# Performance work log

Measured on AMD Instinct MI355X. Metric: run time of the kernel, lower is better.

The kernel has to match this reference:

```python
import jax, jax.numpy as jnp
import numpy as np

MOVING_RATE = 0.999

def _l2norm(x, eps=1e-12):
    # matches F.normalize(dim=-1): x / max(||x||, eps)
    return x / jnp.maximum(jnp.linalg.norm(x, axis=-1, keepdims=True), eps)

def setup_inputs() -> dict:
    k = jax.random.key(0)
    k1, k2, k3 = jax.random.split(k, 3)
    B, S, K, D = 8192, 14, 512, 256
    return {
        "key": jax.random.normal(k1, (B, S, D), dtype=jnp.float32),
        "value": jax.random.normal(k2, (B, S, D), dtype=jnp.float32),
        "memory": jax.random.normal(k3, (S, K, D), dtype=jnp.float32),
    }

def reference(key, value, memory):
    # key, value: (B, S, D); memory: (S, K, D). update=True path, all slots batched.
    K = memory.shape[1]
    xn = _l2norm(key)                                   # (B,S,D)
    mn = _l2norm(memory)                                # (S,K,D)
    score = jnp.einsum('bsd,skd->bsk', xn, mn)          # (B,S,K)

    # --- EMA codebook update (value is detached in the original) ---
    v = jax.lax.stop_gradient(value)
    ind = jnp.argmax(score, axis=-1)                    # (B,S)
    oh = jax.nn.one_hot(ind, K, dtype=value.dtype)      # (B,S,K)
    oh_sum = oh.sum(axis=0)                             # (S,K)
    emb_sum = jnp.einsum('bsd,bsk->skd', v, oh)         # (S,K,D)
    emb_mean = emb_sum / (oh_sum[..., None] + 1e-6)
    new_mem = memory * MOVING_RATE + emb_mean * (1.0 - MOVING_RATE)

    # --- re-score against updated codebook ---
    score2 = jnp.einsum('bsd,skd->bsk', xn, _l2norm(new_mem))
    ind2 = jnp.argmax(score2, axis=-1)
    oh2 = jax.nn.one_hot(ind2, K, dtype=value.dtype)    # (B,S,K)

    # note: original adds value[:, 0, :] (slot 0) for EVERY slot i — kept faithfully
    out = value[:, :1, :] + jnp.einsum('bsk,skd->bsd', oh2, new_mem)  # (B,S,D)
    return out, new_mem
```

## Files before the change

### kernel.cpp

```cpp
#include <hip/hip_runtime.h>
#include <cstddef>
#include <cstdint>

#define B_ 8192
#define S_ 14
#define K_ 512
#define D_ 256

typedef __attribute__((ext_vector_type(8))) short bfx8;
typedef __attribute__((ext_vector_type(4))) float fx4;

typedef __attribute__((address_space(3))) unsigned int       lds_u32;
typedef const __attribute__((address_space(1))) unsigned int glb_u32;

__device__ __forceinline__ void gload16(const void* g, void* l) {
    __builtin_amdgcn_global_load_lds((glb_u32*)g, (lds_u32*)l, 16, 0, 0);
}

__device__ __forceinline__ unsigned short f2bf(float x) {
    union { float f; unsigned int u; } v; v.f = x;
    unsigned int r = (v.u + 0x7FFFu + ((v.u >> 16) & 1u)) >> 16;
    return (unsigned short)r;
}
__device__ __forceinline__ float bf2f(unsigned short h) {
    union { unsigned int u; float f; } v; v.u = ((unsigned int)h) << 16;
    return v.f;
}

__global__ __launch_bounds__(64) void rownorm_kernel(
    const float* __restrict__ rows, float* __restrict__ invn)
{
    const int row  = blockIdx.x;
    const int lane = threadIdx.x;
    const float4 v = *reinterpret_cast<const float4*>(rows + (size_t)row * D_ + lane * 4);
    float ss = v.x * v.x + v.y * v.y + v.z * v.z + v.w * v.w;
    #pragma unroll
    for (int m = 32; m >= 1; m >>= 1) ss += __shfl_xor(ss, m, 64);
    if (lane == 0) invn[row] = 1.0f / fmaxf(sqrtf(ss), 1e-12f);
}

__global__ __launch_bounds__(256) void split_key_kernel(
    const float* __restrict__ key,
    unsigned short* __restrict__ ph, unsigned short* __restrict__ pm,
    unsigned short* __restrict__ pl)
{
    const int gid  = blockIdx.x * 256 + threadIdx.x;
    const int e    = gid * 4;
    const int b    = e / (S_ * D_);
    const int rem  = e - b * (S_ * D_);
    const int s    = rem >> 8;
    const int d    = rem & 255;
    const float4 x = *reinterpret_cast<const float4*>(key + e);
    const size_t o = ((size_t)s * B_ + b) * D_ + d;

    float xs[4] = { x.x, x.y, x.z, x.w };
    unsigned short hh[4], mm[4], ll[4];
    #pragma unroll
    for (int i = 0; i < 4; ++i) {
        unsigned short a = f2bf(xs[i]);
        float r1 = xs[i] - bf2f(a);
        unsigned short bq = f2bf(r1);
        float r2 = r1 - bf2f(bq);
        unsigned short c = f2bf(r2);
        hh[i] = a; mm[i] = bq; ll[i] = c;
    }
    *reinterpret_cast<ushort4*>(ph + o) = make_ushort4(hh[0], hh[1], hh[2], hh[3]);
    *reinterpret_cast<ushort4*>(pm + o) = make_ushort4(mm[0], mm[1], mm[2], mm[3]);
    *reinterpret_cast<ushort4*>(pl + o) = make_ushort4(ll[0], ll[1], ll[2], ll[3]);
}

__global__ __launch_bounds__(256) void split_mem_kernel(
    const float* __restrict__ mem,
    unsigned short* __restrict__ ph, unsigned short* __restrict__ pm,
    unsigned short* __restrict__ pl)
{
    const int e    = (blockIdx.x * 256 + threadIdx.x) * 4;
    const float4 x = *reinterpret_cast<const float4*>(mem + e);
    float xs[4] = { x.x, x.y, x.z, x.w };
    unsigned short hh[4], mm[4], ll[4];
    #pragma unroll
    for (int i = 0; i < 4; ++i) {
        unsigned short a = f2bf(xs[i]);
        float r1 = xs[i] - bf2f(a);
        unsigned short bq = f2bf(r1);
        float r2 = r1 - bf2f(bq);
        unsigned short c = f2bf(r2);
        hh[i] = a; mm[i] = bq; ll[i] = c;
    }
    *reinterpret_cast<ushort4*>(ph + e) = make_ushort4(hh[0], hh[1], hh[2], hh[3]);
    *reinterpret_cast<ushort4*>(pm + e) = make_ushort4(mm[0], mm[1], mm[2], mm[3]);
    *reinterpret_cast<ushort4*>(pl + e) = make_ushort4(ll[0], ll[1], ll[2], ll[3]);
}

__global__ __launch_bounds__(256) void gemm_argmax_kernel(
    const unsigned short* __restrict__ kh, const unsigned short* __restrict__ km,
    const unsigned short* __restrict__ kl,
    const unsigned short* __restrict__ mh, const unsigned short* __restrict__ mm_,
    const unsigned short* __restrict__ ml,
    const float* __restrict__ invn,
    float* __restrict__ pV, int* __restrict__ pI)
{
    __shared__ short T[6][128 * 32];
    __shared__ float sInv[128];
    __shared__ float bV[128][2];
    __shared__ int   bI[128][2];

    const int orig = blockIdx.x;
    const int wg   = (orig & 7) * 448 + (orig >> 3);
    const int by   = wg & 3;
    const int bx   = (wg >> 2) & 63;
    const int s    = wg >> 8;

    const int t    = threadIdx.x;
    const int b0   = bx * 128;
    const int n0   = by * 128;
    const int w    = t >> 6;
    const int lane = t & 63;
    const int wm   = w >> 1, wn = w & 1;
    const int lr   = lane & 15, lg = lane >> 4;

    const size_t sB = (size_t)s * B_;
    const size_t sK = (size_t)s * K_;

    const unsigned short* __restrict__ APl[3] = { kh, km, kl };
    const unsigned short* __restrict__ BPl[3] = { mh, mm_, ml };

    fx4 acc[4][4];
    #pragma unroll
    for (int i = 0; i < 4; ++i)
        #pragma unroll
        for (int j = 0; j < 4; ++j) acc[i][j] = (fx4)0.0f;

    const int rsub = lane >> 2;
    const int csw  = (((lane & 3) ^ ((lane >> 3) & 3)) * 8);
    const int rdof = ((lg ^ ((lr >> 1) & 3)) * 8);

    for (int dc = 0; dc < 8; ++dc) {
        const int dco = dc * 32 + csw;
        #pragma unroll
        for (int p = 0; p < 3; ++p) {
            #pragma unroll
            for (int u = 0; u < 2; ++u) {
                const int R0 = w * 32 + u * 16;
                gload16(APl[p] + (sB + b0 + R0 + rsub) * D_ + dco, &T[p][R0 * 32]);
                gload16(BPl[p] + (sK + n0 + R0 + rsub) * D_ + dco, &T[3 + p][R0 * 32]);
            }
        }
        __syncthreads();

        #pragma unroll
        for (int ap = 0; ap < 3; ++ap) {
            bfx8 af[4];
            #pragma unroll
            for (int i = 0; i < 4; ++i)
                af[i] = *reinterpret_cast<const bfx8*>(
                    &T[ap][(wm * 64 + i * 16 + lr) * 32 + rdof]);
            #pragma unroll
            for (int bp = 0; bp < 3 - ap; ++bp) {
                bfx8 bfr[4];
                #pragma unroll
                for (int j = 0; j < 4; ++j)
                    bfr[j] = *reinterpret_cast<const bfx8*>(
                        &T[3 + bp][(wn * 64 + j * 16 + lr) * 32 + rdof]);
                __builtin_amdgcn_s_setprio(1);
                #pragma unroll
                for (int i = 0; i < 4; ++i)
                    #pragma unroll
                    for (int j = 0; j < 4; ++j)
                        acc[i][j] = __builtin_amdgcn_mfma_f32_16x16x32_bf16(
                            af[i], bfr[j], acc[i][j], 0, 0, 0);
                __builtin_amdgcn_s_setprio(0);
            }
        }
        __syncthreads();
    }

    if (t < 128) sInv[t] = invn[sK + n0 + t];
    __syncthreads();

    #pragma unroll
    for (int i = 0; i < 4; ++i) {
        #pragma unroll
        for (int r = 0; r < 4; ++r) {
            float bv = -3.4e38f; int bi = 0x7fffffff;
            #pragma unroll
            for (int j = 0; j < 4; ++j) {
                const int kloc = wn * 64 + j * 16 + lr;
                const float v  = acc[i][j][r] * sInv[kloc];
                const int  kg  = n0 + kloc;
                if (v > bv || (v == bv && kg < bi)) { bv = v; bi = kg; }
            }
            #pragma unroll
            for (int msk = 1; msk < 16; msk <<= 1) {
                const float ov = __shfl_xor(bv, msk, 64);
                const int   oi = __shfl_xor(bi, msk, 64);
                if (ov > bv || (ov == bv && oi < bi)) { bv = ov; bi = oi; }
            }
            if (lr == 0) {
                const int mrow = wm * 64 + i * 16 + lg * 4 + r;
                bV[mrow][wn] = bv; bI[mrow][wn] = bi;
            }
        }
    }
    __syncthreads();

    if (t < 128) {
        const float v0 = bV[t][0], v1 = bV[t][1];
        const int   i0 = bI[t][0], i1 = bI[t][1];
        const bool take1 = (v1 > v0) || (v1 == v0 && i1 < i0);
        const size_t o = ((size_t)s * 4 + by) * B_ + b0 + t;
        pV[o] = take1 ? v1 : v0;
        pI[o] = take1 ? i1 : i0;
    }
}

__global__ __launch_bounds__(256) void combine1_kernel(
    const float* __restrict__ pV, const int* __restrict__ pI,
    int* __restrict__ ind1)
{
    const int idx = blockIdx.x * 256 + threadIdx.x;
    const int s   = idx >> 13;
    const int b   = idx & 8191;
    float bv = -3.4e38f; int bi = 0x7fffffff;
    #pragma unroll
    for (int nb = 0; nb < 4; ++nb) {
        const size_t o = ((size_t)s * 4 + nb) * B_ + b;
        const float v = pV[o]; const int i = pI[o];
        if (v > bv || (v == bv && i < bi)) { bv = v; bi = i; }
    }
    ind1[idx] = bi;
}

__global__ __launch_bounds__(256) void combine2_out_kernel(
    const float* __restrict__ pV, const int* __restrict__ pI,
    const float* __restrict__ value, const float* __restrict__ newmem,
    float* __restrict__ out)
{
    const int row  = blockIdx.x * 4 + (threadIdx.x >> 6);
    const int lane = threadIdx.x & 63;
    const int s    = row >> 13;
    const int b    = row & 8191;
    float bv = -3.4e38f; int bi = 0x7fffffff;
    #pragma unroll
    for (int nb = 0; nb < 4; ++nb) {
        const size_t o = ((size_t)s * 4 + nb) * B_ + b;
        const float v = pV[o]; const int i = pI[o];
        if (v > bv || (v == bv && i < bi)) { bv = v; bi = i; }
    }
    const float4 vv = *reinterpret_cast<const float4*>(
        value + (size_t)b * (S_ * D_) + lane * 4);
    const float4 mmv = *reinterpret_cast<const float4*>(
        newmem + ((size_t)s * K_ + bi) * D_ + lane * 4);
    float4 o4;
    o4.x = vv.x + mmv.x; o4.y = vv.y + mmv.y;
    o4.z = vv.z + mmv.z; o4.w = vv.w + mmv.w;
    *reinterpret_cast<float4*>(out + ((size_t)b * S_ + s) * D_ + lane * 4) = o4;
}

__global__ __launch_bounds__(256) void u1_hist_kernel(
    const int* __restrict__ ind1, int* __restrict__ hist)
{
    __shared__ int h[K_];
    const int t = threadIdx.x, c = blockIdx.x, s = blockIdx.y;
    h[t] = 0; h[t + 256] = 0;
    __syncthreads();
    const int k = ind1[(size_t)s * B_ + c * 256 + t];
    atomicAdd(&h[k], 1);
    __syncthreads();
    hist[((size_t)s * 32 + c) * K_ + t]       = h[t];
    hist[((size_t)s * 32 + c) * K_ + t + 256] = h[t + 256];
}

__global__ __launch_bounds__(512) void u2_scan_kernel(
    int* __restrict__ hist, int* __restrict__ cnt, int* __restrict__ offs)
{
    __shared__ int sc[K_];
    const int k = threadIdx.x, s = blockIdx.x;
    int run = 0;
    for (int c = 0; c < 32; ++c) {
        const size_t o = ((size_t)s * 32 + c) * K_ + k;
        const int x = hist[o];
        hist[o] = run;
        run += x;
    }
    cnt[s * K_ + k] = run;
    sc[k] = run;
    __syncthreads();
    for (int off = 1; off < K_; off <<= 1) {
        int v = (k >= off) ? sc[k - off] : 0;
        __syncthreads();
        sc[k] += v;
        __syncthreads();
    }
    offs[s * K_ + k] = sc[k] - run;
}

__global__ __launch_bounds__(256) void u3_scatter_kernel(
    const int* __restrict__ ind1, const int* __restrict__ hist,
    const int* __restrict__ offs, int* __restrict__ csr)
{
    __shared__ int sk[256];
    const int t = threadIdx.x, c = blockIdx.x, s = blockIdx.y;
    const int b = c * 256 + t;
    const int k = ind1[(size_t)s * B_ + b];
    sk[t] = k;
    __syncthreads();
    int rank = 0;
    for (int j = 0; j < t; ++j) rank += (sk[j] == k);
    const int pos = offs[s * K_ + k] + hist[((size_t)s * 32 + c) * K_ + k] + rank;
    csr[(size_t)s * B_ + pos] = b;
}

__global__ __launch_bounds__(64) void u4_gather_kernel(
    const int* __restrict__ csr, const int* __restrict__ cnt,
    const int* __restrict__ offs, const float* __restrict__ value,
    const float* __restrict__ memory, float* __restrict__ newmem)
{
    const int k = blockIdx.x, s = blockIdx.y, lane = threadIdx.x;
    const int n = cnt[s * K_ + k];
    const int base = offs[s * K_ + k];
    float4 a; a.x = a.y = a.z = a.w = 0.0f;
    for (int i = 0; i < n; ++i) {
        const int b = csr[(size_t)s * B_ + base + i];
        const float4 v = *reinterpret_cast<const float4*>(
            value + ((size_t)b * S_ + s) * D_ + lane * 4);
        a.x += v.x; a.y += v.y; a.z += v.z; a.w += v.w;
    }
    const float inv = 1.0f / ((float)n + 1e-6f);
    const size_t o = ((size_t)s * K_ + k) * D_ + lane * 4;
    const float4 mo = *reinterpret_cast<const float4*>(memory + o);
    float4 r;
    r.x = mo.x * 0.999f + a.x * inv * 0.001f;
    r.y = mo.y * 0.999f + a.y * inv * 0.001f;
    r.z = mo.z * 0.999f + a.z * inv * 0.001f;
    r.w = mo.w * 0.999f + a.w * inv * 0.001f;
    *reinterpret_cast<float4*>(newmem + o) = r;
}

template <int MODE>
__global__ __launch_bounds__(256) void score_argmax_kernel(
    const float* __restrict__ key, const float* __restrict__ mem,
    const float* __restrict__ invn, const float* __restrict__ value,
    float* __restrict__ out, int* __restrict__ ind_out)
{
    __shared__ __align__(16) float kt[64][36];
    __shared__ __align__(16) float mt[64][36];
    __shared__ float redV[64][16];
    __shared__ int   redI[64][16];

    const int t  = threadIdx.x;
    const int s  = blockIdx.y;
    const int b0 = blockIdx.x * 64;
    const int tb = t & 15;
    const int tk = t >> 4;

    float best[4]; int bidx[4];
    #pragma unroll
    for (int i = 0; i < 4; ++i) { best[i] = -3.4e38f; bidx[i] = 0; }

    for (int kc = 0; kc < 8; ++kc) {
        float acc[4][4];
        #pragma unroll
        for (int i = 0; i < 4; ++i)
            #pragma unroll
            for (int j = 0; j < 4; ++j) acc[i][j] = 0.0f;

        for (int dc = 0; dc < 8; ++dc) {
            #pragma unroll
            for (int u = 0; u < 2; ++u) {
                const int f = t + u * 256;
                const int row = f >> 3;
                const int c4 = f & 7;
                *reinterpret_cast<float4*>(&kt[row][c4 * 4]) =
                    *reinterpret_cast<const float4*>(
                        key + (((size_t)(b0 + row)) * S_ + s) * D_ + dc * 32 + c4 * 4);
                *reinterpret_cast<float4*>(&mt[row][c4 * 4]) =
                    *reinterpret_cast<const float4*>(
                        mem + (((size_t)s * K_) + kc * 64 + row) * D_ + dc * 32 + c4 * 4);
            }
            __syncthreads();
            #pragma unroll
            for (int d4 = 0; d4 < 8; ++d4) {
                float4 a[4], b[4];
                #pragma unroll
                for (int i = 0; i < 4; ++i)
                    a[i] = *reinterpret_cast<const float4*>(&kt[tb + i * 16][d4 * 4]);
                #pragma unroll
                for (int j = 0; j < 4; ++j)
                    b[j] = *reinterpret_cast<const float4*>(&mt[tk + j * 16][d4 * 4]);
                #pragma unroll
                for (int i = 0; i < 4; ++i)
                    #pragma unroll
                    for (int j = 0; j < 4; ++j)
                        acc[i][j] += a[i].x * b[j].x + a[i].y * b[j].y +
                                     a[i].z * b[j].z + a[i].w * b[j].w;
            }
            __syncthreads();
        }
        #pragma unroll
        for (int j = 0; j < 4; ++j) {
            const int kabs = kc * 64 + tk + j * 16;
            const float inv = invn[s * K_ + kabs];
            #pragma unroll
            for (int i = 0; i < 4; ++i) {
                const float v = acc[i][j] * inv;
                if (v > best[i] || (v == best[i] && kabs < bidx[i])) {
                    best[i] = v; bidx[i] = kabs;
                }
            }
        }
    }
    #pragma unroll
    for (int i = 0; i < 4; ++i) {
        redV[tb + i * 16][tk] = best[i];
        redI[tb + i * 16][tk] = bidx[i];
    }
    __syncthreads();
    if (t < 64) {
        float bv = redV[t][0]; int bi = redI[t][0];
        #pragma unroll
        for (int g = 1; g < 16; ++g) {
            const float v = redV[t][g]; const int ix = redI[t][g];
            if (v > bv || (v == bv && ix < bi)) { bv = v; bi = ix; }
        }
        if (MODE == 0) ind_out[(size_t)s * B_ + b0 + t] = bi;
        else           redI[t][0] = bi;
    }
    if (MODE == 1) {
        __syncthreads();
        const int w = t >> 6, lane = t & 63;
        for (int r = w; r < 64; r += 4) {
            const int bg = b0 + r;
            const int kk = redI[r][0];
            const float4 vv = *reinterpret_cast<const float4*>(
                value + (size_t)bg * (S_ * D_) + lane * 4);
            const float4 mmv = *reinterpret_cast<const float4*>(
                mem + ((size_t)s * K_ + kk) * D_ + lane * 4);
            float4 o;
            o.x = vv.x + mmv.x; o.y = vv.y + mmv.y;
            o.z = vv.z + mmv.z; o.w = vv.w + mmv.w;
            *reinterpret_cast<float4*>(
                out + (((size_t)bg) * S_ + s) * D_ + lane * 4) = o;
        }
    }
}

__global__ __launch_bounds__(256) void update_kernel(
    const int* __restrict__ ind1, const float* __restrict__ value,
    const float* __restrict__ memory, float* __restrict__ newmem)
{
    const int k0 = blockIdx.x * 4, s = blockIdx.y, t = threadIdx.x;
    __shared__ int sIdx[256];
    float a0 = 0.f, a1 = 0.f, a2 = 0.f, a3 = 0.f;
    int c0 = 0, c1 = 0, c2 = 0, c3 = 0;
    for (int b0 = 0; b0 < B_; b0 += 256) {
        sIdx[t] = ind1[(size_t)s * B_ + b0 + t];
        __syncthreads();
        for (int bb = 0; bb < 256; ++bb) {
            const int ix = sIdx[bb];
            const unsigned r = (unsigned)(ix - k0);
            if (r < 4u) {
                const float v = value[(((size_t)(b0 + bb)) * S_ + s) * D_ + t];
                if      (r == 0u) { a0 += v; ++c0; }
                else if (r == 1u) { a1 += v; ++c1; }
                else if (r == 2u) { a2 += v; ++c2; }
                else              { a3 += v; ++c3; }
            }
        }
        __syncthreads();
    }
    const float accs[4] = { a0, a1, a2, a3 };
    const int   cns [4] = { c0, c1, c2, c3 };
    #pragma unroll
    for (int kk = 0; kk < 4; ++kk) {
        const size_t off = ((size_t)s * K_ + k0 + kk) * D_ + t;
        const float mean = accs[kk] / ((float)cns[kk] + 1e-6f);
        newmem[off] = memory[off] * 0.999f + mean * 0.001f;
    }
}

extern "C" void kernel_launch(void* const* d_in, const int* in_sizes, int n_in,
                              void* d_out, int out_size, void* d_ws, size_t ws_size,
                              hipStream_t stream)
{
    const float* key    = (const float*)d_in[0];
    const float* value  = (const float*)d_in[1];
    const float* memory = (const float*)d_in[2];

    float* out    = (float*)d_out;
    float* newmem = out + (size_t)B_ * S_ * D_;

    const size_t keyPlane = (size_t)S_ * B_ * D_;
    const size_t memPlane = (size_t)S_ * K_ * D_;
    char* p = (char*)d_ws;
    size_t need = 0;
    auto alloc = [&](size_t bytes) -> char* {
        char* r = p + need;
        need += (bytes + 255) & ~(size_t)255;
        return r;
    };
    unsigned short* kh  = (unsigned short*)alloc(keyPlane * 2);
    unsigned short* km  = (unsigned short*)alloc(keyPlane * 2);
    unsigned short* kl  = (unsigned short*)alloc(keyPlane * 2);
    unsigned short* mh  = (unsigned short*)alloc(memPlane * 2);
    unsigned short* mm  = (unsigned short*)alloc(memPlane * 2);
    unsigned short* ml  = (unsigned short*)alloc(memPlane * 2);
    float* invn   = (float*)alloc((size_t)S_ * K_ * 4);
    float* pV     = (float*)alloc((size_t)S_ * 4 * B_ * 4);
    int*   pI     = (int*)  alloc((size_t)S_ * 4 * B_ * 4);
    int*   ind1   = (int*)  alloc((size_t)S_ * B_ * 4);
    int*   hist   = (int*)  alloc((size_t)S_ * 32 * K_ * 4);
    int*   cnt    = (int*)  alloc((size_t)S_ * K_ * 4);
    int*   offs   = (int*)  alloc((size_t)S_ * K_ * 4);
    int*   csr    = (int*)  alloc((size_t)S_ * B_ * 4);

    if (ws_size >= need) {
        split_key_kernel<<<dim3((B_ * S_ * D_) / 1024), 256, 0, stream>>>(key, kh, km, kl);
        split_mem_kernel<<<dim3((S_ * K_ * D_) / 1024), 256, 0, stream>>>(memory, mh, mm, ml);
        rownorm_kernel<<<dim3(S_ * K_), 64, 0, stream>>>(memory, invn);

        gemm_argmax_kernel<<<dim3(3584), 256, 0, stream>>>(
            kh, km, kl, mh, mm, ml, invn, pV, pI);
        combine1_kernel<<<dim3((S_ * B_) / 256), 256, 0, stream>>>(pV, pI, ind1);

        u1_hist_kernel<<<dim3(32, S_), 256, 0, stream>>>(ind1, hist);
        u2_scan_kernel<<<dim3(S_), 512, 0, stream>>>(hist, cnt, offs);
        u3_scatter_kernel<<<dim3(32, S_), 256, 0, stream>>>(ind1, hist, offs, csr);
        u4_gather_kernel<<<dim3(K_, S_), 64, 0, stream>>>(csr, cnt, offs, value, memory, newmem);

        rownorm_kernel<<<dim3(S_ * K_), 64, 0, stream>>>(newmem, invn);
        split_mem_kernel<<<dim3((S_ * K_ * D_) / 1024), 256, 0, stream>>>(newmem, mh, mm, ml);

        gemm_argmax_kernel<<<dim3(3584), 256, 0, stream>>>(
            kh, km, kl, mh, mm, ml, invn, pV, pI);
        combine2_out_kernel<<<dim3((S_ * B_) / 4), 256, 0, stream>>>(
            pV, pI, value, newmem, out);
    } else {
        float* invn1 = (float*)d_ws;
        float* invn2 = invn1 + S_ * K_;
        int*   find1 = (int*)(invn2 + S_ * K_);

        rownorm_kernel<<<dim3(S_ * K_), 64, 0, stream>>>(memory, invn1);
        score_argmax_kernel<0><<<dim3(B_ / 64, S_), 256, 0, stream>>>(
            key, memory, invn1, nullptr, nullptr, find1);
        update_kernel<<<dim3(K_ / 4, S_), 256, 0, stream>>>(find1, value, memory, newmem);
        rownorm_kernel<<<dim3(S_ * K_), 64, 0, stream>>>(newmem, invn2);
        score_argmax_kernel<1><<<dim3(B_ / 64, S_), 256, 0, stream>>>(
            key, newmem, invn2, value, out, nullptr);
    }
}
```

Baseline: 542.5 us.

## Double-buffer LDS tiles and enlarge GEMM M-tile to 256 rows

```diff
diff --git a/kernel.cpp b/kernel.cpp
--- a/kernel.cpp
+++ b/kernel.cpp
@@ -92,7 +92,7 @@
     *reinterpret_cast<ushort4*>(pl + e) = make_ushort4(ll[0], ll[1], ll[2], ll[3]);
 }
 
-__global__ __launch_bounds__(256) void gemm_argmax_kernel(
+__global__ __launch_bounds__(256, 1) void gemm_argmax_kernel(
     const unsigned short* __restrict__ kh, const unsigned short* __restrict__ km,
     const unsigned short* __restrict__ kl,
     const unsigned short* __restrict__ mh, const unsigned short* __restrict__ mm_,
@@ -100,19 +100,16 @@
     const float* __restrict__ invn,
     float* __restrict__ pV, int* __restrict__ pI)
 {
-    __shared__ short T[6][128 * 32];
-    __shared__ float sInv[128];
-    __shared__ float bV[128][2];
-    __shared__ int   bI[128][2];
+    __shared__ __align__(16) short T[2][36864];
 
     const int orig = blockIdx.x;
-    const int wg   = (orig & 7) * 448 + (orig >> 3);
+    const int wg   = (orig & 7) * 224 + (orig >> 3);
     const int by   = wg & 3;
-    const int bx   = (wg >> 2) & 63;
-    const int s    = wg >> 8;
+    const int bx   = (wg >> 2) & 31;
+    const int s    = wg >> 7;
 
     const int t    = threadIdx.x;
-    const int b0   = bx * 128;
+    const int b0   = bx * 256;
     const int n0   = by * 128;
     const int w    = t >> 6;
     const int lane = t & 63;
@@ -125,9 +122,9 @@
     const unsigned short* __restrict__ APl[3] = { kh, km, kl };
     const unsigned short* __restrict__ BPl[3] = { mh, mm_, ml };
 
-    fx4 acc[4][4];
-    #pragma unroll
-    for (int i = 0; i < 4; ++i)
+    fx4 acc[8][4];
+    #pragma unroll
+    for (int i = 0; i < 8; ++i)
         #pragma unroll
         for (int j = 0; j < 4; ++j) acc[i][j] = (fx4)0.0f;
 
@@ -135,51 +132,71 @@
     const int csw  = (((lane & 3) ^ ((lane >> 3) & 3)) * 8);
     const int rdof = ((lg ^ ((lr >> 1) & 3)) * 8);
 
-    for (int dc = 0; dc < 8; ++dc) {
-        const int dco = dc * 32 + csw;
+    auto stage = [&](int nb, int dcv) {
+        const int dco = dcv * 32 + csw;
         #pragma unroll
         for (int p = 0; p < 3; ++p) {
+            #pragma unroll
+            for (int u = 0; u < 4; ++u) {
+                const int R0 = w * 64 + u * 16;
+                gload16(APl[p] + (sB + b0 + R0 + rsub) * D_ + dco,
+                        &T[nb][p * 8192 + R0 * 32]);
+            }
             #pragma unroll
             for (int u = 0; u < 2; ++u) {
                 const int R0 = w * 32 + u * 16;
-                gload16(APl[p] + (sB + b0 + R0 + rsub) * D_ + dco, &T[p][R0 * 32]);
-                gload16(BPl[p] + (sK + n0 + R0 + rsub) * D_ + dco, &T[3 + p][R0 * 32]);
-            }
-        }
-        __syncthreads();
-
+                gload16(BPl[p] + (sK + n0 + R0 + rsub) * D_ + dco,
+                        &T[nb][24576 + p * 4096 + R0 * 32]);
+            }
+        }
+    };
+
+    stage(0, 0);
+    __syncthreads();
+
+    #pragma unroll 2
+    for (int dc = 0; dc < 8; ++dc) {
+        if (dc < 7) stage((dc + 1) & 1, dc + 1);
+        const short* Tb = &T[dc & 1][0];
+
+        bfx8 bf[3][4];
         #pragma unroll
         for (int ap = 0; ap < 3; ++ap) {
-            bfx8 af[4];
-            #pragma unroll
-            for (int i = 0; i < 4; ++i)
+            bfx8 af[8];
+            #pragma unroll
+            for (int i = 0; i < 8; ++i)
                 af[i] = *reinterpret_cast<const bfx8*>(
-                    &T[ap][(wm * 64 + i * 16 + lr) * 32 + rdof]);
+                    &Tb[ap * 8192 + (wm * 128 + i * 16 + lr) * 32 + rdof]);
             #pragma unroll
             for (int bp = 0; bp < 3 - ap; ++bp) {
-                bfx8 bfr[4];
-                #pragma unroll
-                for (int j = 0; j < 4; ++j)
-                    bfr[j] = *reinterpret_cast<const bfx8*>(
-                        &T[3 + bp][(wn * 64 + j * 16 + lr) * 32 + rdof]);
+                if (ap == 0) {
+                    #pragma unroll
+                    for (int j = 0; j < 4; ++j)
+                        bf[bp][j] = *reinterpret_cast<const bfx8*>(
+                            &Tb[24576 + bp * 4096 + (wn * 64 + j * 16 + lr) * 32 + rdof]);
+                }
                 __builtin_amdgcn_s_setprio(1);
                 #pragma unroll
-                for (int i = 0; i < 4; ++i)
+                for (int i = 0; i < 8; ++i)
                     #pragma unroll
                     for (int j = 0; j < 4; ++j)
                         acc[i][j] = __builtin_amdgcn_mfma_f32_16x16x32_bf16(
-                            af[i], bfr[j], acc[i][j], 0, 0, 0);
+                            af[i], bf[bp][j], acc[i][j], 0, 0, 0);
                 __builtin_amdgcn_s_setprio(0);
             }
         }
         __syncthreads();
     }
 
+    float* sInv = reinterpret_cast<float*>(&T[0][0]);
+    float* bVp  = sInv + 128;
+    int*   bIp  = reinterpret_cast<int*>(bVp + 512);
+
     if (t < 128) sInv[t] = invn[sK + n0 + t];
     __syncthreads();
 
     #pragma unroll
-    for (int i = 0; i < 4; ++i) {
+    for (int i = 0; i < 8; ++i) {
         #pragma unroll
         for (int r = 0; r < 4; ++r) {
             float bv = -3.4e38f; int bi = 0x7fffffff;
@@ -197,16 +214,16 @@
                 if (ov > bv || (ov == bv && oi < bi)) { bv = ov; bi = oi; }
             }
             if (lr == 0) {
-                const int mrow = wm * 64 + i * 16 + lg * 4 + r;
-                bV[mrow][wn] = bv; bI[mrow][wn] = bi;
-            }
-        }
-    }
-    __syncthreads();
-
-    if (t < 128) {
-        const float v0 = bV[t][0], v1 = bV[t][1];
-        const int   i0 = bI[t][0], i1 = bI[t][1];
+                const int mrow = wm * 128 + i * 16 + lg * 4 + r;
+                bVp[mrow * 2 + wn] = bv; bIp[mrow * 2 + wn] = bi;
+            }
+        }
+    }
+    __syncthreads();
+
+    {
+        const float v0 = bVp[t * 2], v1 = bVp[t * 2 + 1];
+        const int   i0 = bIp[t * 2], i1 = bIp[t * 2 + 1];
         const bool take1 = (v1 > v0) || (v1 == v0 && i1 < i0);
         const size_t o = ((size_t)s * 4 + by) * B_ + b0 + t;
         pV[o] = take1 ? v1 : v0;
@@ -519,7 +536,7 @@
         split_mem_kernel<<<dim3((S_ * K_ * D_) / 1024), 256, 0, stream>>>(memory, mh, mm, ml);
         rownorm_kernel<<<dim3(S_ * K_), 64, 0, stream>>>(memory, invn);
 
-        gemm_argmax_kernel<<<dim3(3584), 256, 0, stream>>>(
+        gemm_argmax_kernel<<<dim3(1792), 256, 0, stream>>>(
             kh, km, kl, mh, mm, ml, invn, pV, pI);
         combine1_kernel<<<dim3((S_ * B_) / 256), 256, 0, stream>>>(pV, pI, ind1);
 
@@ -531,7 +548,7 @@
         rownorm_kernel<<<dim3(S_ * K_), 64, 0, stream>>>(newmem, invn);
         split_mem_kernel<<<dim3((S_ * K_ * D_) / 1024), 256, 0, stream>>>(newmem, mh, mm, ml);
 
-        gemm_argmax_kernel<<<dim3(3584), 256, 0, stream>>>(
+        gemm_argmax_kernel<<<dim3(1792), 256, 0, stream>>>(
             kh, km, kl, mh, mm, ml, invn, pV, pI);
         combine2_out_kernel<<<dim3((S_ * B_) / 4), 256, 0, stream>>>(
             pV, pI, value, newmem, out);
```

Measured after the change: 694.5 us. +28.0%, slower.

## Enlarge GEMM tile to 256 rows with 512 threads and fuse memory split with row norm

Applied to the files above, without the earlier changes.

```diff
diff --git a/kernel.cpp b/kernel.cpp
--- a/kernel.cpp
+++ b/kernel.cpp
@@ -69,13 +69,16 @@
     *reinterpret_cast<ushort4*>(pl + o) = make_ushort4(ll[0], ll[1], ll[2], ll[3]);
 }
 
-__global__ __launch_bounds__(256) void split_mem_kernel(
+__global__ __launch_bounds__(64) void splitnorm_mem_kernel(
     const float* __restrict__ mem,
     unsigned short* __restrict__ ph, unsigned short* __restrict__ pm,
-    unsigned short* __restrict__ pl)
-{
-    const int e    = (blockIdx.x * 256 + threadIdx.x) * 4;
+    unsigned short* __restrict__ pl, float* __restrict__ invn)
+{
+    const int row  = blockIdx.x;
+    const int lane = threadIdx.x;
+    const size_t e = (size_t)row * D_ + lane * 4;
     const float4 x = *reinterpret_cast<const float4*>(mem + e);
+
     float xs[4] = { x.x, x.y, x.z, x.w };
     unsigned short hh[4], mm[4], ll[4];
     #pragma unroll
@@ -90,9 +93,14 @@
     *reinterpret_cast<ushort4*>(ph + e) = make_ushort4(hh[0], hh[1], hh[2], hh[3]);
     *reinterpret_cast<ushort4*>(pm + e) = make_ushort4(mm[0], mm[1], mm[2], mm[3]);
     *reinterpret_cast<ushort4*>(pl + e) = make_ushort4(ll[0], ll[1], ll[2], ll[3]);
-}
-
-__global__ __launch_bounds__(256) void gemm_argmax_kernel(
+
+    float ss = x.x * x.x + x.y * x.y + x.z * x.z + x.w * x.w;
+    #pragma unroll
+    for (int m = 32; m >= 1; m >>= 1) ss += __shfl_xor(ss, m, 64);
+    if (lane == 0) invn[row] = 1.0f / fmaxf(sqrtf(ss), 1e-12f);
+}
+
+__global__ __launch_bounds__(512, 4) void gemm_argmax_kernel(
     const unsigned short* __restrict__ kh, const unsigned short* __restrict__ km,
     const unsigned short* __restrict__ kl,
     const unsigned short* __restrict__ mh, const unsigned short* __restrict__ mm_,
@@ -100,23 +108,21 @@
     const float* __restrict__ invn,
     float* __restrict__ pV, int* __restrict__ pI)
 {
-    __shared__ short T[6][128 * 32];
-    __shared__ float sInv[128];
-    __shared__ float bV[128][2];
-    __shared__ int   bI[128][2];
+    __shared__ __align__(16) short T[36864];
 
     const int orig = blockIdx.x;
-    const int wg   = (orig & 7) * 448 + (orig >> 3);
+    const int wg   = (orig & 7) * 224 + (orig >> 3);
     const int by   = wg & 3;
-    const int bx   = (wg >> 2) & 63;
-    const int s    = wg >> 8;
+    const int bx   = (wg >> 2) & 31;
+    const int s    = wg >> 7;
 
     const int t    = threadIdx.x;
-    const int b0   = bx * 128;
+    const int b0   = bx * 256;
     const int n0   = by * 128;
     const int w    = t >> 6;
     const int lane = t & 63;
-    const int wm   = w >> 1, wn = w & 1;
+    const int wm   = w >> 1;
+    const int wn   = w & 1;
     const int lr   = lane & 15, lg = lane >> 4;
 
     const size_t sB = (size_t)s * B_;
@@ -142,8 +148,13 @@
             #pragma unroll
             for (int u = 0; u < 2; ++u) {
                 const int R0 = w * 32 + u * 16;
-                gload16(APl[p] + (sB + b0 + R0 + rsub) * D_ + dco, &T[p][R0 * 32]);
-                gload16(BPl[p] + (sK + n0 + R0 + rsub) * D_ + dco, &T[3 + p][R0 * 32]);
+                gload16(APl[p] + (sB + b0 + R0 + rsub) * D_ + dco,
+                        &T[p * 8192 + R0 * 32]);
+            }
+            {
+                const int R0 = w * 16;
+                gload16(BPl[p] + (sK + n0 + R0 + rsub) * D_ + dco,
+                        &T[24576 + p * 4096 + R0 * 32]);
             }
         }
         __syncthreads();
@@ -154,14 +165,14 @@
             #pragma unroll
             for (int i = 0; i < 4; ++i)
                 af[i] = *reinterpret_cast<const bfx8*>(
-                    &T[ap][(wm * 64 + i * 16 + lr) * 32 + rdof]);
+                    &T[ap * 8192 + (wm * 64 + i * 16 + lr) * 32 + rdof]);
             #pragma unroll
             for (int bp = 0; bp < 3 - ap; ++bp) {
                 bfx8 bfr[4];
                 #pragma unroll
                 for (int j = 0; j < 4; ++j)
                     bfr[j] = *reinterpret_cast<const bfx8*>(
-                        &T[3 + bp][(wn * 64 + j * 16 + lr) * 32 + rdof]);
+                        &T[24576 + bp * 4096 + (wn * 64 + j * 16 + lr) * 32 + rdof]);
                 __builtin_amdgcn_s_setprio(1);
                 #pragma unroll
                 for (int i = 0; i < 4; ++i)
@@ -175,6 +186,10 @@
         __syncthreads();
     }
 
+    float* sInv = reinterpret_cast<float*>(&T[0]);
+    float* bVp  = sInv + 128;
+    int*   bIp  = reinterpret_cast<int*>(bVp + 512);
+
     if (t < 128) sInv[t] = invn[sK + n0 + t];
     __syncthreads();
 
@@ -198,15 +213,15 @@
             }
             if (lr == 0) {
                 const int mrow = wm * 64 + i * 16 + lg * 4 + r;
-                bV[mrow][wn] = bv; bI[mrow][wn] = bi;
-            }
-        }
-    }
-    __syncthreads();
-
-    if (t < 128) {
-        const float v0 = bV[t][0], v1 = bV[t][1];
-        const int   i0 = bI[t][0], i1 = bI[t][1];
+                bVp[mrow * 2 + wn] = bv; bIp[mrow * 2 + wn] = bi;
+            }
+        }
+    }
+    __syncthreads();
+
+    if (t < 256) {
+        const float v0 = bVp[t * 2], v1 = bVp[t * 2 + 1];
+        const int   i0 = bIp[t * 2], i1 = bIp[t * 2 + 1];
         const bool take1 = (v1 > v0) || (v1 == v0 && i1 < i0);
         const size_t o = ((size_t)s * 4 + by) * B_ + b0 + t;
         pV[o] = take1 ? v1 : v0;
@@ -516,10 +531,9 @@
 
     if (ws_size >= need) {
         split_key_kernel<<<dim3((B_ * S_ * D_) / 1024), 256, 0, stream>>>(key, kh, km, kl);
-        split_mem_kernel<<<dim3((S_ * K_ * D_) / 1024), 256, 0, stream>>>(memory, mh, mm, ml);
-        rownorm_kernel<<<dim3(S_ * K_), 64, 0, stream>>>(memory, invn);
-
-        gemm_argmax_kernel<<<dim3(3584), 256, 0, stream>>>(
+        splitnorm_mem_kernel<<<dim3(S_ * K_), 64, 0, stream>>>(memory, mh, mm, ml, invn);
+
+        gemm_argmax_kernel<<<dim3(1792), 512, 0, stream>>>(
             kh, km, kl, mh, mm, ml, invn, pV, pI);
         combine1_kernel<<<dim3((S_ * B_) / 256), 256, 0, stream>>>(pV, pI, ind1);
 
@@ -528,10 +542,9 @@
         u3_scatter_kernel<<<dim3(32, S_), 256, 0, stream>>>(ind1, hist, offs, csr);
         u4_gather_kernel<<<dim3(K_, S_), 64, 0, stream>>>(csr, cnt, offs, value, memory, newmem);
 
-        rownorm_kernel<<<dim3(S_ * K_), 64, 0, stream>>>(newmem, invn);
-        split_mem_kernel<<<dim3((S_ * K_ * D_) / 1024), 256, 0, stream>>>(newmem, mh, mm, ml);
-
-        gemm_argmax_kernel<<<dim3(3584), 256, 0, stream>>>(
+        splitnorm_mem_kernel<<<dim3(S_ * K_), 64, 0, stream>>>(newmem, mh, mm, ml, invn);
+
+        gemm_argmax_kernel<<<dim3(1792), 512, 0, stream>>>(
             kh, km, kl, mh, mm, ml, invn, pV, pI);
         combine2_out_kernel<<<dim3((S_ * B_) / 4), 256, 0, stream>>>(
             pV, pI, value, newmem, out);
```

Result: faster. 459.3 us (-15.3%).
